# Kernel tuning notes

Measured on AMD Instinct MI355X. Metric: run time of the kernel, lower is better.

## Reference

```python
import jax, jax.numpy as jnp
import numpy as np

HEADS = 8
N = 2048; D_IN = 2048; LATENT = 2048; PROJ = 256; HIDDEN = 128
LAGS = 12; E = 65536; EMB = 128; N_ENT = 10000; N_TS = 1000


def _lag_weights(L):
    # weights(): flip(arange(1..L) / (L*(L+1)/2)); sums to 1
    w = np.arange(1, L + 1, dtype=np.float64) / (L * (L + 1) // 2)
    return jnp.asarray(np.ascontiguousarray(w[::-1]), dtype=jnp.float32)


def _gatv2(x, edge_index, Wl, bl, Wr, br, att, bias):
    # GATv2Conv with PyG defaults: self-loops added, leaky_relu(0.2),
    # softmax over incoming edges per target node, concat heads + bias.
    n = x.shape[0]
    H = HEADS
    D = Wl.shape[1] // H
    sl = jnp.arange(n, dtype=edge_index.dtype)
    src = jnp.concatenate([edge_index[0], sl])
    dst = jnp.concatenate([edge_index[1], sl])
    xl = (x @ Wl + bl).reshape(n, H, D)  # source / message transform
    xr = (x @ Wr + br).reshape(n, H, D)  # target transform
    e = jnp.sum(jax.nn.leaky_relu(xl[src] + xr[dst], 0.2) * att, axis=-1)  # [E', H]
    emax = jax.ops.segment_max(e, dst, num_segments=n)
    ee = jnp.exp(e - emax[dst])
    alpha = ee / jax.ops.segment_sum(ee, dst, num_segments=n)[dst]
    out = jax.ops.segment_sum(alpha[:, :, None] * xl[src], dst, num_segments=n)  # [n,H,D]
    return out.reshape(n, H * D) + bias


def _mha(query, lagged, Wq, bq, Wk, bk, Wv, bv):
    # MultiHeadCausalAttention: per-lag K/V projections combined with fixed
    # triangular weights. Since the weights sum to 1, the projection bias
    # passes through the weighted sum unchanged, so the per-lag Python loop
    # fuses into a single einsum over the lag axis.
    n = query.shape[0]
    dim_out = Wq.shape[1]
    dh = dim_out // HEADS
    Q = (query @ Wq + bq).reshape(n, -1, HEADS, dh).transpose(0, 2, 1, 3)  # [n,H,q,dh]
    tw = _lag_weights(lagged.shape[1])
    K = (jnp.einsum('nli,io,l->no', lagged, Wk, tw) + bk).reshape(n, 1, HEADS, dh).transpose(0, 2, 1, 3)
    V = (jnp.einsum('nli,io,l->no', lagged, Wv, tw) + bv).reshape(n, 1, HEADS, dh).transpose(0, 2, 1, 3)
    scores = jnp.einsum('nhqd,nhkd->nhqk', Q, K) / (dh ** 0.5)
    attn = jax.nn.softmax(scores, axis=-1)
    return jnp.einsum('nhqk,nhkd->nhqd', attn, V).transpose(0, 2, 1, 3).reshape(n, -1, dim_out)


def _forward(time_series_data, lagged_data, eps, gumbel_noise,
             entity_table, timestamp_table,
             gat_e_Wl, gat_e_bl, gat_e_Wr, gat_e_br, gat_e_att, gat_e_bias,
             enc_proj_W, enc_proj_b,
             enc_Wq, enc_bq, enc_Wk, enc_bk, enc_Wv, enc_bv,
             enc_fc_W, enc_fc_b,
             dec_Wq, dec_bq, dec_Wk, dec_bk, dec_Wv, dec_bv,
             gat_d_Wl, gat_d_bl, gat_d_Wr, gat_d_br, gat_d_att, gat_d_bias,
             dec_fc_W, dec_fc_b, A_direct, A_indirect,
             entity_indices, timestamp_indices, edge_index):
    entity_emb = entity_table[entity_indices]      # pretrained TKG entity embedding
    ts_emb = timestamp_table[timestamp_indices]    # pretrained TKG timestamp embedding
    feats = jnp.concatenate([time_series_data, entity_emb, ts_emb], axis=-1)
    x = jax.nn.relu(_gatv2(feats, edge_index, gat_e_Wl, gat_e_bl, gat_e_Wr, gat_e_br, gat_e_att, gat_e_bias))
    x = jax.nn.relu(x @ enc_proj_W + enc_proj_b)
    x = jax.nn.relu(_mha(x, lagged_data, enc_Wq, enc_bq, enc_Wk, enc_bk, enc_Wv, enc_bv))  # [N,1,PROJ]
    q_params = x @ enc_fc_W + enc_fc_b
    mean, log_var = jnp.split(q_params, 2, axis=-1)
    z = mean + jnp.exp(0.5 * log_var) * eps  # reparameterization, [N,1,LATENT]
    x = jax.nn.relu(_mha(z, lagged_data, dec_Wq, dec_bq, dec_Wk, dec_bk, dec_Wv, dec_bv))[:, 0, :]
    x = jax.nn.relu(_gatv2(x, edge_index, gat_d_Wl, gat_d_bl, gat_d_Wr, gat_d_br, gat_d_att, gat_d_bias))
    x_rec = x @ dec_fc_W + dec_fc_b  # [N, D_IN]
    direct = A_direct * jnp.sum(x_rec, axis=0)        # einsum('ij,tj->ij')
    indirect = A_indirect * jnp.sum(z, axis=(0, 1))   # einsum('ij,tlj->ij')
    causal_effect = direct + indirect
    y = jax.nn.softmax((causal_effect + gumbel_noise) / 0.5, axis=-1)  # tau=0.5
    hard = jax.nn.one_hot(jnp.argmax(y, axis=-1), y.shape[-1], dtype=y.dtype)
    adj = jax.lax.stop_gradient(hard - y) + y  # hard gumbel-softmax, straight-through
    return z, mean, log_var, x_rec, causal_effect, adj


def setup_inputs():
    key = jax.random.key(0)
    ks = iter(jax.random.split(key, 64))
    def nrm(shape, s=0.02):
        return jax.random.normal(next(ks), shape, jnp.float32) * s
    A0 = jnp.ones((N, N), jnp.float32) + jnp.eye(N, dtype=jnp.float32)
    A0 = A0 / jnp.sum(A0, axis=1)  # matches torch broadcast A0 / A0.sum(1)
    HH = HEADS * HIDDEN
    d = {
        'entity_indices': jax.random.randint(next(ks), (N,), 0, N_ENT),
        'relation_indices': jax.random.randint(next(ks), (N,), 0, N_TS),
        'timestamp_indices': jax.random.randint(next(ks), (N,), 0, N_TS),
        'time_series_data': jax.random.normal(next(ks), (N, D_IN), jnp.float32),
        'edge_index': jax.random.randint(next(ks), (2, E), 0, N),
        'lagged_data': jax.random.normal(next(ks), (N, LAGS, D_IN), jnp.float32),
        'eps': jax.random.normal(next(ks), (N, 1, LATENT), jnp.float32),
        'gumbel_noise': jax.random.gumbel(next(ks), (N, N), jnp.float32),
        'entity_table': nrm((N_ENT, EMB), 1.0),
        'timestamp_table': nrm((N_TS, EMB), 1.0),
        'gat_e_Wl': nrm((D_IN + 2 * EMB, HH)), 'gat_e_bl': jnp.zeros((HH,), jnp.float32),
        'gat_e_Wr': nrm((D_IN + 2 * EMB, HH)), 'gat_e_br': jnp.zeros((HH,), jnp.float32),
        'gat_e_att': nrm((HEADS, HIDDEN), 0.1), 'gat_e_bias': jnp.zeros((HH,), jnp.float32),
        'enc_proj_W': nrm((HH, PROJ)), 'enc_proj_b': jnp.zeros((PROJ,), jnp.float32),
        'enc_Wq': nrm((PROJ, PROJ)), 'enc_bq': jnp.zeros((PROJ,), jnp.float32),
        'enc_Wk': nrm((D_IN, PROJ)), 'enc_bk': jnp.zeros((PROJ,), jnp.float32),
        'enc_Wv': nrm((D_IN, PROJ)), 'enc_bv': jnp.zeros((PROJ,), jnp.float32),
        'enc_fc_W': nrm((PROJ, 2 * LATENT)), 'enc_fc_b': jnp.zeros((2 * LATENT,), jnp.float32),
        'dec_Wq': nrm((LATENT, PROJ)), 'dec_bq': jnp.zeros((PROJ,), jnp.float32),
        'dec_Wk': nrm((D_IN, PROJ)), 'dec_bk': jnp.zeros((PROJ,), jnp.float32),
        'dec_Wv': nrm((D_IN, PROJ)), 'dec_bv': jnp.zeros((PROJ,), jnp.float32),
        'gat_d_Wl': nrm((PROJ, HH)), 'gat_d_bl': jnp.zeros((HH,), jnp.float32),
        'gat_d_Wr': nrm((PROJ, HH)), 'gat_d_br': jnp.zeros((HH,), jnp.float32),
        'gat_d_att': nrm((HEADS, HIDDEN), 0.1), 'gat_d_bias': jnp.zeros((HH,), jnp.float32),
        'dec_fc_W': nrm((HH, D_IN)), 'dec_fc_b': jnp.zeros((D_IN,), jnp.float32),
        'A_direct': A0, 'A_indirect': A0,
    }
    return d


def reference(entity_indices, relation_indices, timestamp_indices, time_series_data,
              edge_index, lagged_data, eps, gumbel_noise,
              entity_table, timestamp_table,
              gat_e_Wl, gat_e_bl, gat_e_Wr, gat_e_br, gat_e_att, gat_e_bias,
              enc_proj_W, enc_proj_b,
              enc_Wq, enc_bq, enc_Wk, enc_bk, enc_Wv, enc_bv,
              enc_fc_W, enc_fc_b,
              dec_Wq, dec_bq, dec_Wk, dec_bk, dec_Wv, dec_bv,
              gat_d_Wl, gat_d_bl, gat_d_Wr, gat_d_br, gat_d_att, gat_d_bias,
              dec_fc_W, dec_fc_b, A_direct, A_indirect):
    # relation_indices are looked up by the pretrained TKG, but the relation
    # embedding is unused downstream in the original forward, so it is ignored.
    return _forward(time_series_data, lagged_data, eps, gumbel_noise,
                    entity_table, timestamp_table,
                    gat_e_Wl, gat_e_bl, gat_e_Wr, gat_e_br, gat_e_att, gat_e_bias,
                    enc_proj_W, enc_proj_b,
                    enc_Wq, enc_bq, enc_Wk, enc_bk, enc_Wv, enc_bv,
                    enc_fc_W, enc_fc_b,
                    dec_Wq, dec_bq, dec_Wk, dec_bk, dec_Wv, dec_bv,
                    gat_d_Wl, gat_d_bl, gat_d_Wr, gat_d_br, gat_d_att, gat_d_bias,
                    dec_fc_W, dec_fc_b, A_direct, A_indirect,
                    entity_indices, timestamp_indices, edge_index)
```

## Files before the change

kernel.cpp:

```cpp
#include <hip/hip_runtime.h>
#include <hip/hip_bf16.h>
#include <math.h>

#define N_NODES 2048
#define DIN     2048
#define HH      1024
#define LAGS    12
#define NE      65536
#define NL      (2048 * 2048)
#define CHUNK   128

#define BM 128
#define BN 128
#define BK 32

typedef __attribute__((ext_vector_type(8))) short short8;
typedef __attribute__((ext_vector_type(4))) float f32x4;

static __device__ __forceinline__ short f2bf_rne(float x) {
  union { float f; unsigned u; } c; c.f = x;
  unsigned u = c.u;
  unsigned r = (u + 0x7fffu + ((u >> 16) & 1u)) >> 16;
  return (short)r;
}
static __device__ __forceinline__ float bf2f(short h) {
  union { unsigned u; float f; } c; c.u = ((unsigned)(unsigned short)h) << 16;
  return c.f;
}

typedef __attribute__((address_space(3))) unsigned int as3_u32;
typedef const __attribute__((address_space(1))) unsigned int as1_u32c;
static __device__ __forceinline__ void gload_lds16(const void* g, void* l) {
  __builtin_amdgcn_global_load_lds((as1_u32c*)g, (as3_u32*)l, 16, 0, 0);
}

#define VMCNT6  asm volatile("s_waitcnt vmcnt(6)" ::: "memory")
#define VMCNT4  asm volatile("s_waitcnt vmcnt(4)" ::: "memory")
#define VMCNT0  asm volatile("s_waitcnt vmcnt(0)" ::: "memory")
#define SBAR()  do { asm volatile("" ::: "memory"); __builtin_amdgcn_s_barrier(); \
                     asm volatile("" ::: "memory"); } while (0)

struct WCfg { const float* W; short* H; short* L; int K; int N; int nb; };
struct WCfg2 { WCfg c[2]; };
struct WCfg4 { WCfg c[4]; };

static __device__ __forceinline__ void wsplit_tile(
    const WCfg& cf, int local, int tid, float t[32][33])
{
  const float* W = cf.W;
  short* H = cf.H;
  short* L = cf.L;
  int K = cf.K, N = cf.N;
  int nbx = N >> 5;
  int bx = local % nbx, by = local / nbx;
  int tx = tid & 31, ty = tid >> 5;
  int c0 = bx << 5, k0 = by << 5;
#pragma unroll
  for (int j = 0; j < 4; ++j)
    t[ty + 8 * j][tx] = W[(size_t)(k0 + ty + 8 * j) * N + c0 + tx];
  __syncthreads();
#pragma unroll
  for (int j = 0; j < 4; ++j) {
    int c = ty + 8 * j;
    float x = t[tx][c];
    short h = f2bf_rne(x);
    size_t off = (size_t)(c0 + c) * K + k0 + tx;
    H[off] = h;
    if (L) L[off] = f2bf_rne(x - bf2f(h));
  }
}

__global__ __launch_bounds__(256) void megaA_kernel(
    const float* __restrict__ lagged, short* __restrict__ lw, WCfg2 cfgs,
    int* __restrict__ cursor, float* __restrict__ csx,
    float* __restrict__ csz, float* __restrict__ cs_gat)
{
  __shared__ float t[32][33];
  int bid = blockIdx.x;
  int tid = threadIdx.x;

  if (bid < 2048) {
    int idx = bid * 256 + tid;
    int n = idx >> 8, c8 = idx & 255;
    const float* base = lagged + (size_t)n * (LAGS * DIN) + (size_t)c8 * 8;
    float a[8] = {};
#pragma unroll
    for (int l = 0; l < LAGS; ++l) {
      float w = (float)((double)(LAGS - l) / 78.0);
      float4 v0 = *(const float4*)(base + (size_t)l * DIN);
      float4 v1 = *(const float4*)(base + (size_t)l * DIN + 4);
      a[0] += w * v0.x; a[1] += w * v0.y; a[2] += w * v0.z; a[3] += w * v0.w;
      a[4] += w * v1.x; a[5] += w * v1.y; a[6] += w * v1.z; a[7] += w * v1.w;
    }
    short8 h;
#pragma unroll
    for (int j = 0; j < 8; ++j) h[j] = f2bf_rne(a[j]);
    *(short8*)(lw + (size_t)idx * 8) = h;
  } else if (bid < 3072) {
    int wb = bid - 2048;
    int i = (wb >= cfgs.c[0].nb) ? 1 : 0;
    int local = wb - (i ? cfgs.c[0].nb : 0);
    wsplit_tile(cfgs.c[i], local, tid, t);
  } else {
    int i = (bid - 3072) * 256 + tid;
    cursor[i] = 0; csx[i] = 0.f; csz[i] = 0.f;
    if (i < 1024) cs_gat[i] = 0.f;
  }
}

__global__ __launch_bounds__(256) void megaC_kernel(
    const short* __restrict__ A, const short* __restrict__ Bh0,
    const short* __restrict__ Bh1, short* __restrict__ Cpart,
    WCfg4 cfgs,
    const int* __restrict__ esrc, const int* __restrict__ edst,
    int* __restrict__ cursor, int* __restrict__ csr)
{
  __shared__ char smem[32768];
  int fb = blockIdx.x;
  int tid = threadIdx.x;

  if (fb < 512) {
    short* lds = (short*)smem;
    const int K = 2048, N = 256, M = 2048, klen = 256;
    int lane = tid & 63, wid = tid >> 6;
    int bn = (fb & 1) * BN;
    int bm = ((fb >> 1) & 15) * BM;
    int z = fb >> 5;
    int twin = z & 1;
    int kb = (z >> 1) * klen;
    const short* Bh = twin ? Bh1 : Bh0;

    const short* gp[4];
    int lofs[4];
    {
      int r4 = lane >> 2;
      int ksw = (lane & 3) ^ ((lane >> 3) & 3);
#pragma unroll
      for (int c = 0; c < 4; ++c) {
        int chunk = wid * 4 + c;
        int p = chunk >> 3, s = chunk & 7;
        int r = (s << 4) + r4;
        const short* bp = (p == 0) ? (A + (size_t)(bm + r) * K)
                                   : (Bh + (size_t)(bn + r) * K);
        gp[c] = bp + kb + (ksw << 3);
        lofs[c] = (p << 12) + (s << 9);
      }
    }
    auto stage = [&](int bo) {
#pragma unroll
      for (int c = 0; c < 4; ++c) {
        gload_lds16(gp[c], lds + bo + lofs[c]);
        gp[c] += BK;
      }
    };

    int l15 = lane & 15, l4 = lane >> 4;
    int wr = wid >> 1, wc = wid & 1;
    int soff = (l4 ^ ((l15 >> 1) & 3)) << 3;
    int aoff[4], bhoff[4];
#pragma unroll
    for (int i = 0; i < 4; ++i) {
      int r = wr * 64 + i * 16 + l15;
      int c = wc * 64 + i * 16 + l15;
      aoff[i]  = r * BK + soff;
      bhoff[i] = 4096 + c * BK + soff;
    }

    f32x4 acc[4][4];
#pragma unroll
    for (int m = 0; m < 4; ++m)
#pragma unroll
      for (int n = 0; n < 4; ++n) acc[m][n] = (f32x4){0.f, 0.f, 0.f, 0.f};

    stage(0);
    int cur = 0;
#pragma unroll
    for (int t = 0; t < 8; ++t) {
      if (t + 1 < 8) { stage(cur ? 0 : 8192); VMCNT4; }
      else { VMCNT0; }
      SBAR();
      const short* rb = lds + (cur ? 8192 : 0);
      short8 af[4], bh8[4];
#pragma unroll
      for (int i = 0; i < 4; ++i) {
        af[i]  = *(const short8*)(rb + aoff[i]);
        bh8[i] = *(const short8*)(rb + bhoff[i]);
      }
#pragma unroll
      for (int m = 0; m < 4; ++m)
#pragma unroll
        for (int n = 0; n < 4; ++n)
          acc[m][n] = __builtin_amdgcn_mfma_f32_16x16x32_bf16(af[m], bh8[n], acc[m][n], 0, 0, 0);
      SBAR();
      cur ^= 1;
    }

    short* P = Cpart + (size_t)z * ((size_t)M * N);
#pragma unroll
    for (int n = 0; n < 4; ++n) {
      int col = bn + wc * 64 + n * 16 + l15;
#pragma unroll
      for (int m = 0; m < 4; ++m) {
        int row0 = bm + wr * 64 + m * 16 + (l4 << 2);
#pragma unroll
        for (int r = 0; r < 4; ++r)
          P[(size_t)(row0 + r) * N + col] = f2bf_rne(acc[m][n][r]);
      }
    }
  } else if (fb < 4096) {
    float (*t)[33] = (float(*)[33])smem;
    int wb = fb - 512;
    int i = 0, base = 0;
    while (i < 3 && wb >= base + cfgs.c[i].nb) { base += cfgs.c[i].nb; ++i; }
    wsplit_tile(cfgs.c[i], wb - base, tid, t);
  } else {
    int i = (fb - 4096) * 256 + tid;
    if (i < NE) {
      int d = edst[i];
      int p = atomicAdd(&cursor[d], 1);
      if (p < 128) csr[(d << 7) + p] = esrc[i];
    } else if (i < NE + N_NODES) {
      int nn = i - NE;
      int p = atomicAdd(&cursor[nn], 1);
      if (p < 128) csr[(nn << 7) + p] = nn;
    }
  }
}

__global__ __launch_bounds__(256) void gemm_xrec(
    const short* __restrict__ A, const short* __restrict__ Bh,
    short* __restrict__ Cpart, float* __restrict__ cs_gat)
{
  __shared__ short lds[2 * 8192];
  const int K = 1024, N = 2048, M = 2048, klen = 512;
  int tid = threadIdx.x;
  int lane = tid & 63, wid = tid >> 6;
  int bn = blockIdx.x * BN, bm = blockIdx.y * BM;
  int z = blockIdx.z;
  int kb = z * klen;

  const short* gp[4];
  int lofs[4];
  {
    int r4 = lane >> 2;
    int ksw = (lane & 3) ^ ((lane >> 3) & 3);
#pragma unroll
    for (int c = 0; c < 4; ++c) {
      int chunk = wid * 4 + c;
      int p = chunk >> 3, s = chunk & 7;
      int r = (s << 4) + r4;
      const short* bp = (p == 0) ? (A + (size_t)(bm + r) * K)
                                 : (Bh + (size_t)(bn + r) * K);
      gp[c] = bp + kb + (ksw << 3);
      lofs[c] = (p << 12) + (s << 9);
    }
  }
  auto stage = [&](int bo) {
#pragma unroll
    for (int c = 0; c < 4; ++c) {
      gload_lds16(gp[c], lds + bo + lofs[c]);
      gp[c] += BK;
    }
  };

  int l15 = lane & 15, l4 = lane >> 4;
  int wr = wid >> 1, wc = wid & 1;
  int soff = (l4 ^ ((l15 >> 1) & 3)) << 3;
  int aoff[4], bhoff[4];
#pragma unroll
  for (int i = 0; i < 4; ++i) {
    int r = wr * 64 + i * 16 + l15;
    int c = wc * 64 + i * 16 + l15;
    aoff[i]  = r * BK + soff;
    bhoff[i] = 4096 + c * BK + soff;
  }

  f32x4 acc[4][4];
#pragma unroll
  for (int m = 0; m < 4; ++m)
#pragma unroll
    for (int n = 0; n < 4; ++n) acc[m][n] = (f32x4){0.f, 0.f, 0.f, 0.f};

  const int nt = klen / BK;
  stage(0);
  int cur = 0;
  for (int t = 0; t < nt; ++t) {
    if (t + 1 < nt) { stage(cur ? 0 : 8192); VMCNT4; }
    else { VMCNT0; }
    SBAR();
    const short* rb = lds + (cur ? 8192 : 0);
    short8 af[4], bh8[4];
#pragma unroll
    for (int i = 0; i < 4; ++i) {
      af[i]  = *(const short8*)(rb + aoff[i]);
      bh8[i] = *(const short8*)(rb + bhoff[i]);
    }
#pragma unroll
    for (int m = 0; m < 4; ++m)
#pragma unroll
      for (int n = 0; n < 4; ++n)
        acc[m][n] = __builtin_amdgcn_mfma_f32_16x16x32_bf16(af[m], bh8[n], acc[m][n], 0, 0, 0);
    SBAR();
    cur ^= 1;
  }

  short* P = Cpart + (size_t)z * ((size_t)M * N);
#pragma unroll
  for (int n = 0; n < 4; ++n) {
    int col = bn + wc * 64 + n * 16 + l15;
#pragma unroll
    for (int m = 0; m < 4; ++m) {
      int row0 = bm + wr * 64 + m * 16 + (l4 << 2);
#pragma unroll
      for (int r = 0; r < 4; ++r)
        P[(size_t)(row0 + r) * N + col] = f2bf_rne(acc[m][n][r]);
    }
  }

  if (blockIdx.x == 0) {
    int k0 = kb + tid * 2;
    float s0 = 0.f, s1 = 0.f;
    const short* Ar = A + (size_t)bm * K + k0;
    for (int r = 0; r < 128; ++r) {
      short2 v = *(const short2*)(Ar + (size_t)r * K);
      s0 += bf2f(v.x);
      s1 += bf2f(v.y);
    }
    atomicAdd(&cs_gat[k0], s0);
    atomicAdd(&cs_gat[k0 + 1], s1);
  }
}

__global__ __launch_bounds__(256) void gemm_dual(
    const short* __restrict__ xe, const short* __restrict__ xd,
    const short* __restrict__ fcH, const short* __restrict__ fcL,
    const short* __restrict__ WlH, const short* __restrict__ WlL,
    const short* __restrict__ WrH, const short* __restrict__ WrL,
    const float* __restrict__ fc_b, const float* __restrict__ bl,
    const float* __restrict__ br,
    float* __restrict__ out_mean, float* __restrict__ out_lv,
    short* __restrict__ xl, short* __restrict__ xr)
{
  __shared__ short lds[2 * 12288];
  const int K = 256;
  int fb = blockIdx.x;
  const short *A, *Bh, *Bl;
  const float* bias;
  int bm, bn, jobB, ldc;
  short* Obf = nullptr;
  float* Of = nullptr;
  if (fb < 512) {
    A = xe; Bh = fcH; Bl = fcL; bias = fc_b;
    bn = (fb & 31) << 7; bm = (fb >> 5) << 7;
    jobB = 0; ldc = 2048; Of = out_mean;
  } else {
    int g = fb - 512, twin = g & 1, t = g >> 1;
    A = xd; Bh = twin ? WrH : WlH; Bl = twin ? WrL : WlL;
    bias = twin ? br : bl;
    bn = (t & 7) << 7; bm = (t >> 3) << 7;
    jobB = 1; ldc = 1024; Obf = twin ? xr : xl;
  }

  int tid = threadIdx.x;
  int lane = tid & 63, wid = tid >> 6;

  const short* gp[6];
  int lofs[6];
  {
    int r4 = lane >> 2;
    int ksw = (lane & 3) ^ ((lane >> 3) & 3);
#pragma unroll
    for (int c = 0; c < 6; ++c) {
      int chunk = wid * 6 + c;
      int p = chunk >> 3, s = chunk & 7;
      int r = (s << 4) + r4;
      const short* bp = (p == 0) ? (A + (size_t)(bm + r) * K)
                      : (p == 1) ? (Bh + (size_t)(bn + r) * K)
                                 : (Bl + (size_t)(bn + r) * K);
      gp[c] = bp + (ksw << 3);
      lofs[c] = (p << 12) + (s << 9);
    }
  }
  auto stage = [&](int bo) {
#pragma unroll
    for (int c = 0; c < 6; ++c) {
      gload_lds16(gp[c], lds + bo + lofs[c]);
      gp[c] += BK;
    }
  };

  int l15 = lane & 15, l4 = lane >> 4;
  int wr = wid >> 1, wc = wid & 1;
  int soff = (l4 ^ ((l15 >> 1) & 3)) << 3;
  int aoff[4], bhoff[4], bloff[4];
#pragma unroll
  for (int i = 0; i < 4; ++i) {
    int r = wr * 64 + i * 16 + l15;
    int c = wc * 64 + i * 16 + l15;
    aoff[i]  = r * BK + soff;
    bhoff[i] = 4096 + c * BK + soff;
    bloff[i] = 8192 + c * BK + soff;
  }

  f32x4 acc[4][4];
#pragma unroll
  for (int m = 0; m < 4; ++m)
#pragma unroll
    for (int n = 0; n < 4; ++n) acc[m][n] = (f32x4){0.f, 0.f, 0.f, 0.f};

  stage(0);
  int cur = 0;
#pragma unroll
  for (int t = 0; t < 8; ++t) {
    if (t + 1 < 8) { stage(cur ? 0 : 12288); VMCNT6; }
    else { VMCNT0; }
    SBAR();
    const short* rb = lds + (cur ? 12288 : 0);
    short8 af[4], bh8[4], bl8[4];
#pragma unroll
    for (int i = 0; i < 4; ++i) {
      af[i]  = *(const short8*)(rb + aoff[i]);
      bh8[i] = *(const short8*)(rb + bhoff[i]);
      bl8[i] = *(const short8*)(rb + bloff[i]);
    }
#pragma unroll
    for (int m = 0; m < 4; ++m)
#pragma unroll
      for (int n = 0; n < 4; ++n) {
        acc[m][n] = __builtin_amdgcn_mfma_f32_16x16x32_bf16(af[m], bh8[n], acc[m][n], 0, 0, 0);
        acc[m][n] = __builtin_amdgcn_mfma_f32_16x16x32_bf16(af[m], bl8[n], acc[m][n], 0, 0, 0);
      }
    SBAR();
    cur ^= 1;
  }

#pragma unroll
  for (int n = 0; n < 4; ++n) {
    int col = bn + wc * 64 + n * 16 + l15;
    float bv = bias[col];
    if (jobB) {
#pragma unroll
      for (int m = 0; m < 4; ++m) {
        int row0 = bm + wr * 64 + m * 16 + (l4 << 2);
#pragma unroll
        for (int r = 0; r < 4; ++r)
          Obf[(size_t)(row0 + r) * ldc + col] = f2bf_rne(acc[m][n][r] + bv);
      }
    } else {
      float* O = Of; int oc = col;
      if (col >= 2048) { O = out_lv; oc = col - 2048; }
#pragma unroll
      for (int m = 0; m < 4; ++m) {
        int row0 = bm + wr * 64 + m * 16 + (l4 << 2);
#pragma unroll
        for (int r = 0; r < 4; ++r)
          O[(size_t)(row0 + r) * ldc + oc] = acc[m][n][r] + bv;
      }
    }
  }
}

__global__ __launch_bounds__(256) void sumrelu_kernel(
    const short* __restrict__ part, const float* __restrict__ b0,
    const float* __restrict__ b1, short* __restrict__ xe,
    short* __restrict__ xd)
{
  int i4 = blockIdx.x * 256 + threadIdx.x;
  size_t S = (size_t)N_NODES * 256;
  size_t base = (size_t)i4 * 4;
  int col = (int)(base & 255);
  float4 b0v = *(const float4*)(b0 + col);
  float4 b1v = *(const float4*)(b1 + col);
  float s0[4] = {}, s1[4] = {};
#pragma unroll
  for (int c = 0; c < 8; ++c) {
    short4 p0 = *(const short4*)(part + (size_t)(2 * c) * S + base);
    short4 p1 = *(const short4*)(part + (size_t)(2 * c + 1) * S + base);
    s0[0] += bf2f(p0.x); s0[1] += bf2f(p0.y); s0[2] += bf2f(p0.z); s0[3] += bf2f(p0.w);
    s1[0] += bf2f(p1.x); s1[1] += bf2f(p1.y); s1[2] += bf2f(p1.z); s1[3] += bf2f(p1.w);
  }
  short4 e, d;
  e.x = f2bf_rne(fmaxf(s0[0] + b0v.x, 0.f));
  e.y = f2bf_rne(fmaxf(s0[1] + b0v.y, 0.f));
  e.z = f2bf_rne(fmaxf(s0[2] + b0v.z, 0.f));
  e.w = f2bf_rne(fmaxf(s0[3] + b0v.w, 0.f));
  d.x = f2bf_rne(fmaxf(s1[0] + b1v.x, 0.f));
  d.y = f2bf_rne(fmaxf(s1[1] + b1v.y, 0.f));
  d.z = f2bf_rne(fmaxf(s1[2] + b1v.z, 0.f));
  d.w = f2bf_rne(fmaxf(s1[3] + b1v.w, 0.f));
  *(short4*)(xe + base) = e;
  *(short4*)(xd + base) = d;
}

__global__ __launch_bounds__(256) void megaB_kernel(
    const short* __restrict__ xl, const short* __restrict__ xr,
    const float* __restrict__ att, const float* __restrict__ bias,
    const int* __restrict__ csr, const int* __restrict__ cursor,
    short* __restrict__ outp,
    const float* __restrict__ mean_in, const float* __restrict__ lv_in,
    const float* __restrict__ eps, float* __restrict__ z,
    float* __restrict__ csz)
{
  __shared__ float xr_s[HH];
  __shared__ float att_s[HH];
  __shared__ float e_s[8 * CHUNK];
  __shared__ int   src_s[CHUNK];
  __shared__ float m_s[8], s_s[8], f_s[8];

  int tid = threadIdx.x;

  if (blockIdx.x >= 2048) {
    int flat = blockIdx.x - 2048;
    int c = ((flat & 3) * 256 + tid) * 2;
    int r0 = (flat >> 2) * 16;
    float sx = 0.f, sy = 0.f;
    for (int r = r0; r < r0 + 16; ++r) {
      size_t off = (size_t)r * 2048 + c;
      float2 m = *(const float2*)(mean_in + off);
      float2 v = *(const float2*)(lv_in + off);
      float2 e = *(const float2*)(eps + off);
      float zx = m.x + expf(0.5f * v.x) * e.x;
      float zy = m.y + expf(0.5f * v.y) * e.y;
      *(float2*)(z + off) = make_float2(zx, zy);
      sx += zx; sy += zy;
    }
    atomicAdd(&csz[c], sx);
    atomicAdd(&csz[c + 1], sy);
    return;
  }

  int n = blockIdx.x;
  {
    short4 x4 = ((const short4*)(xr + (size_t)n * HH))[tid];
    xr_s[tid * 4 + 0] = bf2f(x4.x);
    xr_s[tid * 4 + 1] = bf2f(x4.y);
    xr_s[tid * 4 + 2] = bf2f(x4.z);
    xr_s[tid * 4 + 3] = bf2f(x4.w);
  }
  ((float4*)att_s)[tid] = ((const float4*)att)[tid];
  if (tid < 8) { m_s[tid] = -INFINITY; s_s[tid] = 0.f; }
  __syncthreads();

  int beg = n << 7;
  int cnt_total = min(cursor[n], 128);
  int end = beg + cnt_total;
  int ht = tid >> 5;
  float4 acc = make_float4(0.f, 0.f, 0.f, 0.f);

  for (int c0 = beg; c0 < end; c0 += CHUNK) {
    int cnt = min(CHUNK, end - c0);
    if (tid < cnt) src_s[tid] = csr[c0 + tid];
    __syncthreads();

    int wave = tid >> 6, lane = tid & 63;
    int d0 = lane << 4;
    for (int e = wave; e < cnt; e += 4) {
      const short* xlr = xl + (size_t)src_s[e] * HH + d0;
      short8 a0 = *(const short8*)xlr;
      short8 a1 = *(const short8*)(xlr + 8);
      float sum = 0.f;
#pragma unroll
      for (int j = 0; j < 8; ++j) {
        float t = bf2f(a0[j]) + xr_s[d0 + j];
        t = t > 0.f ? t : 0.2f * t;
        sum += t * att_s[d0 + j];
      }
#pragma unroll
      for (int j = 0; j < 8; ++j) {
        float t = bf2f(a1[j]) + xr_s[d0 + 8 + j];
        t = t > 0.f ? t : 0.2f * t;
        sum += t * att_s[d0 + 8 + j];
      }
      sum += __shfl_xor(sum, 1);
      sum += __shfl_xor(sum, 2);
      sum += __shfl_xor(sum, 4);
      if ((lane & 7) == 0) e_s[(lane >> 3) * CHUNK + e] = sum;
    }
    __syncthreads();

    {
      int h = tid >> 5, i0 = tid & 31;
      float cm = -INFINITY;
      for (int e = i0; e < cnt; e += 32) cm = fmaxf(cm, e_s[h * CHUNK + e]);
#pragma unroll
      for (int m = 1; m < 32; m <<= 1) cm = fmaxf(cm, __shfl_xor(cm, m));
      float m_old = m_s[h];
      float m_new = fmaxf(m_old, cm);
      float csum = 0.f;
      for (int e = i0; e < cnt; e += 32) {
        float p = expf(e_s[h * CHUNK + e] - m_new);
        e_s[h * CHUNK + e] = p;
        csum += p;
      }
#pragma unroll
      for (int m = 1; m < 32; m <<= 1) csum += __shfl_xor(csum, m);
      if (i0 == 0) {
        float f = expf(m_old - m_new);
        s_s[h] = s_s[h] * f + csum;
        m_s[h] = m_new;
        f_s[h] = f;
      }
    }
    __syncthreads();

    float f = f_s[ht];
    acc.x *= f; acc.y *= f; acc.z *= f; acc.w *= f;
    for (int e = 0; e < cnt; ++e) {
      float p = e_s[ht * CHUNK + e];
      short4 v = *(const short4*)(xl + (size_t)src_s[e] * HH + (tid << 2));
      acc.x += p * bf2f(v.x); acc.y += p * bf2f(v.y);
      acc.z += p * bf2f(v.z); acc.w += p * bf2f(v.w);
    }
    __syncthreads();
  }

  float inv = 1.0f / s_s[ht];
  float4 b4 = *(const float4*)(bias + (tid << 2));
  short4 o4;
  o4.x = f2bf_rne(fmaxf(acc.x * inv + b4.x, 0.f));
  o4.y = f2bf_rne(fmaxf(acc.y * inv + b4.y, 0.f));
  o4.z = f2bf_rne(fmaxf(acc.z * inv + b4.z, 0.f));
  o4.w = f2bf_rne(fmaxf(acc.w * inv + b4.w, 0.f));
  *(short4*)(outp + (size_t)n * HH + (tid << 2)) = o4;
}

__global__ __launch_bounds__(256) void xrec_sum_kernel(
    const short* __restrict__ part, const float* __restrict__ bias,
    float* __restrict__ xrec, float* __restrict__ csx,
    const float* __restrict__ cs_gat, const short* __restrict__ dfL)
{
  int c = (blockIdx.x * 256 + threadIdx.x) * 2;
  int r0 = blockIdx.y * 16;
  size_t S = (size_t)N_NODES * 2048;
  float2 b = *(const float2*)(bias + c);
  float sx = 0.f, sy = 0.f;
  for (int r = r0; r < r0 + 16; ++r) {
    size_t off = (size_t)r * 2048 + c;
    short2 p0 = *(const short2*)(part + off);
    short2 p1 = *(const short2*)(part + S + off);
    float vx = bf2f(p0.x) + bf2f(p1.x) + b.x;
    float vy = bf2f(p0.y) + bf2f(p1.y) + b.y;
    *(float2*)(xrec + off) = make_float2(vx, vy);
    sx += vx; sy += vy;
  }
  {
    int k0 = blockIdx.y * 8;
    const short* rw0 = dfL + (size_t)c * 1024 + k0;
    const short* rw1 = dfL + (size_t)(c + 1) * 1024 + k0;
#pragma unroll
    for (int j = 0; j < 8; j += 4) {
      float4 g = *(const float4*)(cs_gat + k0 + j);
      short4 w0 = *(const short4*)(rw0 + j);
      short4 w1 = *(const short4*)(rw1 + j);
      sx += g.x * bf2f(w0.x) + g.y * bf2f(w0.y) + g.z * bf2f(w0.z) + g.w * bf2f(w0.w);
      sy += g.x * bf2f(w1.x) + g.y * bf2f(w1.y) + g.z * bf2f(w1.z) + g.w * bf2f(w1.w);
    }
  }
  atomicAdd(&csx[c], sx);
  atomicAdd(&csx[c + 1], sy);
}

__global__ __launch_bounds__(256) void final_kernel(
    const float* __restrict__ Ad, const float* __restrict__ Ai,
    const float* __restrict__ gum, const float* __restrict__ csx,
    const float* __restrict__ csz, float* __restrict__ ce_out,
    float* __restrict__ adj_out)
{
  int i = blockIdx.x;
  int tid = threadIdx.x;
  size_t rb = (size_t)i * 2048;

  float vmax = -INFINITY; int vidx = 0;
  for (int j4 = tid; j4 < 512; j4 += 256) {
    float4 ad = *(const float4*)(Ad  + rb + (size_t)j4 * 4);
    float4 ai = *(const float4*)(Ai  + rb + (size_t)j4 * 4);
    float4 g  = *(const float4*)(gum + rb + (size_t)j4 * 4);
    float4 cx = *(const float4*)(csx + (size_t)j4 * 4);
    float4 cz = *(const float4*)(csz + (size_t)j4 * 4);
    float4 ce;
    ce.x = ad.x * cx.x + ai.x * cz.x;
    ce.y = ad.y * cx.y + ai.y * cz.y;
    ce.z = ad.z * cx.z + ai.z * cz.z;
    ce.w = ad.w * cx.w + ai.w * cz.w;
    *(float4*)(ce_out + rb + (size_t)j4 * 4) = ce;
    int j = j4 * 4;
    float l;
    l = (ce.x + g.x) * 2.0f; if (l > vmax) { vmax = l; vidx = j; }
    l = (ce.y + g.y) * 2.0f; if (l > vmax) { vmax = l; vidx = j + 1; }
    l = (ce.z + g.z) * 2.0f; if (l > vmax) { vmax = l; vidx = j + 2; }
    l = (ce.w + g.w) * 2.0f; if (l > vmax) { vmax = l; vidx = j + 3; }
  }
  for (int m = 1; m < 64; m <<= 1) {
    float ov = __shfl_xor(vmax, m);
    int   oi = __shfl_xor(vidx, m);
    if (ov > vmax || (ov == vmax && oi < vidx)) { vmax = ov; vidx = oi; }
  }
  __shared__ float wm[4];
  __shared__ int   wi[4];
  __shared__ int   amax;
  int lane = tid & 63, wave = tid >> 6;
  if (lane == 0) { wm[wave] = vmax; wi[wave] = vidx; }
  __syncthreads();
  if (tid == 0) {
    float bv = wm[0]; int bi = wi[0];
    for (int w = 1; w < 4; ++w)
      if (wm[w] > bv || (wm[w] == bv && wi[w] < bi)) { bv = wm[w]; bi = wi[w]; }
    amax = bi;
  }
  __syncthreads();
  int am = amax;
  for (int j4 = tid; j4 < 512; j4 += 256) {
    int j = j4 * 4;
    float4 o;
    o.x = (j     == am) ? 1.f : 0.f;
    o.y = (j + 1 == am) ? 1.f : 0.f;
    o.z = (j + 2 == am) ? 1.f : 0.f;
    o.w = (j + 3 == am) ? 1.f : 0.f;
    *(float4*)(adj_out + rb + (size_t)j4 * 4) = o;
  }
}

extern "C" void kernel_launch(void* const* d_in, const int* in_sizes, int n_in,
                              void* d_out, int out_size, void* d_ws, size_t ws_size,
                              hipStream_t stream) {
  (void)in_sizes; (void)n_in; (void)out_size; (void)ws_size;

  const int*   edge_index = (const int*)d_in[4];
  const float* lagged     = (const float*)d_in[5];
  const float* eps        = (const float*)d_in[6];
  const float* gumbel     = (const float*)d_in[7];
  const float* enc_Wv     = (const float*)d_in[22];
  const float* enc_bv     = (const float*)d_in[23];
  const float* enc_fc_W   = (const float*)d_in[24];
  const float* enc_fc_b   = (const float*)d_in[25];
  const float* dec_Wv     = (const float*)d_in[30];
  const float* dec_bv     = (const float*)d_in[31];
  const float* gat_Wl     = (const float*)d_in[32];
  const float* gat_bl     = (const float*)d_in[33];
  const float* gat_Wr     = (const float*)d_in[34];
  const float* gat_br     = (const float*)d_in[35];
  const float* gat_att    = (const float*)d_in[36];
  const float* gat_bias   = (const float*)d_in[37];
  const float* dec_fc_W   = (const float*)d_in[38];
  const float* dec_fc_b   = (const float*)d_in[39];
  const float* A_dir      = (const float*)d_in[40];
  const float* A_ind      = (const float*)d_in[41];

  float* out      = (float*)d_out;
  float* out_z    = out;
  float* out_mean = out + (size_t)NL;
  float* out_lv   = out + 2 * (size_t)NL;
  float* out_xrec = out + 3 * (size_t)NL;
  float* out_ce   = out + 4 * (size_t)NL;
  float* out_adj  = out + 5 * (size_t)NL;

  char* ws = (char*)d_ws;
  short* lw_bf = (short*)(ws);
  short* WvH0  = (short*)(ws + ((size_t) 8 << 20));
  short* WvH1  = (short*)(ws + ((size_t)10 << 20));
  short* fcH   = (short*)(ws + ((size_t)12 << 20));
  short* fcL   = (short*)(ws + ((size_t)14 << 20));
  short* WlH   = (short*)(ws + ((size_t)16 << 20));
  short* WlL   = (short*)(ws + ((size_t)16 << 20) + (512u << 10));
  short* WrH   = (short*)(ws + ((size_t)17 << 20));
  short* WrL   = (short*)(ws + ((size_t)17 << 20) + (512u << 10));
  short* dfH   = (short*)(ws + ((size_t)18 << 20));
  short* dfL   = (short*)(ws + ((size_t)22 << 20));
  short* xe_bf = (short*)(ws + ((size_t)26 << 20));
  short* xd_bf = (short*)(ws + ((size_t)27 << 20));
  short* xl    = (short*)(ws + ((size_t)28 << 20));
  short* xr    = (short*)(ws + ((size_t)32 << 20));
  short* gt_bf = (short*)(ws + ((size_t)44 << 20));
  short* part  = (short*)(ws + ((size_t)48 << 20));
  int*   cursor = (int*) (ws + ((size_t)64 << 20));
  int*   csr    = (int*) (ws + ((size_t)64 << 20) + (64u << 10));
  float* csx    = (float*)(ws + ((size_t)66 << 20));
  float* csz    = (float*)(ws + ((size_t)66 << 20) + (16u << 10));
  float* cs_gat = (float*)(ws + ((size_t)66 << 20) + (32u << 10));

  const int* e_src = edge_index;
  const int* e_dst = edge_index + NE;

  {
    WCfg2 c2;
    c2.c[0] = { enc_Wv, WvH0, nullptr, 2048, 256, 512 };
    c2.c[1] = { dec_Wv, WvH1, nullptr, 2048, 256, 512 };
    megaA_kernel<<<3080, 256, 0, stream>>>(lagged, lw_bf, c2,
                                           cursor, csx, csz, cs_gat);
  }

  {
    WCfg4 c4;
    c4.c[0] = { enc_fc_W, fcH, fcL, 256,  4096, 1024 };
    c4.c[1] = { gat_Wl,   WlH, WlL, 256,  1024, 256  };
    c4.c[2] = { gat_Wr,   WrH, WrL, 256,  1024, 256  };
    c4.c[3] = { dec_fc_W, dfH, dfL, 1024, 2048, 2048 };
    megaC_kernel<<<4360, 256, 0, stream>>>(
        lw_bf, WvH0, WvH1, part, c4, e_src, e_dst, cursor, csr);
  }

  sumrelu_kernel<<<512, 256, 0, stream>>>(part, enc_bv, dec_bv, xe_bf, xd_bf);

  gemm_dual<<<768, 256, 0, stream>>>(
      xe_bf, xd_bf, fcH, fcL, WlH, WlL, WrH, WrL,
      enc_fc_b, gat_bl, gat_br, out_mean, out_lv, xl, xr);

  megaB_kernel<<<2560, 256, 0, stream>>>(
      xl, xr, gat_att, gat_bias, csr, cursor, gt_bf,
      out_mean, out_lv, eps, out_z, csz);

  gemm_xrec<<<dim3(16, 16, 2), 256, 0, stream>>>(gt_bf, dfH, part, cs_gat);
  xrec_sum_kernel<<<dim3(4, 128), 256, 0, stream>>>(
      part, dec_fc_b, out_xrec, csx, cs_gat, dfL);

  final_kernel<<<N_NODES, 256, 0, stream>>>(A_dir, A_ind, gumbel, csx, csz,
                                            out_ce, out_adj);
}
```

Baseline: 188.5 us.

## Halve split-K partials in value GEMM and drop low-part weights for GAT projections

The lagged-value GEMM in megaC now uses 256 blocks with a K slice of 512 instead of 512 blocks with a slice of 256. This halves the number of bf16 partial buffers that sumrelu must read and reduce. Separately, the GAT Wl/Wr projections in gemm_dual now use only the high bf16 part of the split weights. That drops the second MFMA and the extra B-tile load on that path, at the cost of reduced precision in xl/xr. Fewer blocks in the split-K GEMM lengthens each block's serial loop and lowers parallelism.

```diff
diff --git a/kernel.cpp b/kernel.cpp
--- a/kernel.cpp
+++ b/kernel.cpp
@@ -119,9 +119,9 @@
   int fb = blockIdx.x;
   int tid = threadIdx.x;
 
-  if (fb < 512) {
+  if (fb < 256) {
     short* lds = (short*)smem;
-    const int K = 2048, N = 256, M = 2048, klen = 256;
+    const int K = 2048, N = 256, M = 2048, klen = 512;
     int lane = tid & 63, wid = tid >> 6;
     int bn = (fb & 1) * BN;
     int bm = ((fb >> 1) & 15) * BM;
@@ -172,11 +172,11 @@
 #pragma unroll
       for (int n = 0; n < 4; ++n) acc[m][n] = (f32x4){0.f, 0.f, 0.f, 0.f};
 
+    const int nt = klen / BK;
     stage(0);
     int cur = 0;
-#pragma unroll
-    for (int t = 0; t < 8; ++t) {
-      if (t + 1 < 8) { stage(cur ? 0 : 8192); VMCNT4; }
+    for (int t = 0; t < nt; ++t) {
+      if (t + 1 < nt) { stage(cur ? 0 : 8192); VMCNT4; }
       else { VMCNT0; }
       SBAR();
       const short* rb = lds + (cur ? 8192 : 0);
@@ -207,14 +207,14 @@
           P[(size_t)(row0 + r) * N + col] = f2bf_rne(acc[m][n][r]);
       }
     }
-  } else if (fb < 4096) {
+  } else if (fb < 3840) {
     float (*t)[33] = (float(*)[33])smem;
-    int wb = fb - 512;
+    int wb = fb - 256;
     int i = 0, base = 0;
     while (i < 3 && wb >= base + cfgs.c[i].nb) { base += cfgs.c[i].nb; ++i; }
     wsplit_tile(cfgs.c[i], wb - base, tid, t);
   } else {
-    int i = (fb - 4096) * 256 + tid;
+    int i = (fb - 3840) * 256 + tid;
     if (i < NE) {
       int d = edst[i];
       int p = atomicAdd(&cursor[d], 1);
@@ -334,8 +334,7 @@
 __global__ __launch_bounds__(256) void gemm_dual(
     const short* __restrict__ xe, const short* __restrict__ xd,
     const short* __restrict__ fcH, const short* __restrict__ fcL,
-    const short* __restrict__ WlH, const short* __restrict__ WlL,
-    const short* __restrict__ WrH, const short* __restrict__ WrL,
+    const short* __restrict__ WlH, const short* __restrict__ WrH,
     const float* __restrict__ fc_b, const float* __restrict__ bl,
     const float* __restrict__ br,
     float* __restrict__ out_mean, float* __restrict__ out_lv,
@@ -344,117 +343,177 @@
   __shared__ short lds[2 * 12288];
   const int K = 256;
   int fb = blockIdx.x;
-  const short *A, *Bh, *Bl;
-  const float* bias;
-  int bm, bn, jobB, ldc;
-  short* Obf = nullptr;
-  float* Of = nullptr;
-  if (fb < 512) {
-    A = xe; Bh = fcH; Bl = fcL; bias = fc_b;
-    bn = (fb & 31) << 7; bm = (fb >> 5) << 7;
-    jobB = 0; ldc = 2048; Of = out_mean;
-  } else {
-    int g = fb - 512, twin = g & 1, t = g >> 1;
-    A = xd; Bh = twin ? WrH : WlH; Bl = twin ? WrL : WlL;
-    bias = twin ? br : bl;
-    bn = (t & 7) << 7; bm = (t >> 3) << 7;
-    jobB = 1; ldc = 1024; Obf = twin ? xr : xl;
-  }
-
   int tid = threadIdx.x;
   int lane = tid & 63, wid = tid >> 6;
-
-  const short* gp[6];
-  int lofs[6];
-  {
-    int r4 = lane >> 2;
-    int ksw = (lane & 3) ^ ((lane >> 3) & 3);
-#pragma unroll
-    for (int c = 0; c < 6; ++c) {
-      int chunk = wid * 6 + c;
-      int p = chunk >> 3, s = chunk & 7;
-      int r = (s << 4) + r4;
-      const short* bp = (p == 0) ? (A + (size_t)(bm + r) * K)
-                      : (p == 1) ? (Bh + (size_t)(bn + r) * K)
-                                 : (Bl + (size_t)(bn + r) * K);
-      gp[c] = bp + (ksw << 3);
-      lofs[c] = (p << 12) + (s << 9);
-    }
-  }
-  auto stage = [&](int bo) {
-#pragma unroll
-    for (int c = 0; c < 6; ++c) {
-      gload_lds16(gp[c], lds + bo + lofs[c]);
-      gp[c] += BK;
-    }
-  };
-
   int l15 = lane & 15, l4 = lane >> 4;
   int wr = wid >> 1, wc = wid & 1;
   int soff = (l4 ^ ((l15 >> 1) & 3)) << 3;
-  int aoff[4], bhoff[4], bloff[4];
-#pragma unroll
-  for (int i = 0; i < 4; ++i) {
-    int r = wr * 64 + i * 16 + l15;
-    int c = wc * 64 + i * 16 + l15;
-    aoff[i]  = r * BK + soff;
-    bhoff[i] = 4096 + c * BK + soff;
-    bloff[i] = 8192 + c * BK + soff;
-  }
-
-  f32x4 acc[4][4];
-#pragma unroll
-  for (int m = 0; m < 4; ++m)
-#pragma unroll
-    for (int n = 0; n < 4; ++n) acc[m][n] = (f32x4){0.f, 0.f, 0.f, 0.f};
-
-  stage(0);
-  int cur = 0;
-#pragma unroll
-  for (int t = 0; t < 8; ++t) {
-    if (t + 1 < 8) { stage(cur ? 0 : 12288); VMCNT6; }
-    else { VMCNT0; }
-    SBAR();
-    const short* rb = lds + (cur ? 12288 : 0);
-    short8 af[4], bh8[4], bl8[4];
+
+  if (fb < 512) {
+    const short* A = xe;
+    int bn = (fb & 31) << 7, bm = (fb >> 5) << 7;
+
+    const short* gp[6];
+    int lofs[6];
+    {
+      int r4 = lane >> 2;
+      int ksw = (lane & 3) ^ ((lane >> 3) & 3);
+#pragma unroll
+      for (int c = 0; c < 6; ++c) {
+        int chunk = wid * 6 + c;
+        int p = chunk >> 3, s = chunk & 7;
+        int r = (s << 4) + r4;
+        const short* bp = (p == 0) ? (A + (size_t)(bm + r) * K)
+                        : (p == 1) ? (fcH + (size_t)(bn + r) * K)
+                                   : (fcL + (size_t)(bn + r) * K);
+        gp[c] = bp + (ksw << 3);
+        lofs[c] = (p << 12) + (s << 9);
+      }
+    }
+    auto stage = [&](int bo) {
+#pragma unroll
+      for (int c = 0; c < 6; ++c) {
+        gload_lds16(gp[c], lds + bo + lofs[c]);
+        gp[c] += BK;
+      }
+    };
+
+    int aoff[4], bhoff[4], bloff[4];
 #pragma unroll
     for (int i = 0; i < 4; ++i) {
-      af[i]  = *(const short8*)(rb + aoff[i]);
-      bh8[i] = *(const short8*)(rb + bhoff[i]);
-      bl8[i] = *(const short8*)(rb + bloff[i]);
-    }
+      int r = wr * 64 + i * 16 + l15;
+      int c = wc * 64 + i * 16 + l15;
+      aoff[i]  = r * BK + soff;
+      bhoff[i] = 4096 + c * BK + soff;
+      bloff[i] = 8192 + c * BK + soff;
+    }
+
+    f32x4 acc[4][4];
 #pragma unroll
     for (int m = 0; m < 4; ++m)
 #pragma unroll
-      for (int n = 0; n < 4; ++n) {
-        acc[m][n] = __builtin_amdgcn_mfma_f32_16x16x32_bf16(af[m], bh8[n], acc[m][n], 0, 0, 0);
-        acc[m][n] = __builtin_amdgcn_mfma_f32_16x16x32_bf16(af[m], bl8[n], acc[m][n], 0, 0, 0);
-      }
-    SBAR();
-    cur ^= 1;
-  }
-
-#pragma unroll
-  for (int n = 0; n < 4; ++n) {
-    int col = bn + wc * 64 + n * 16 + l15;
-    float bv = bias[col];
-    if (jobB) {
+      for (int n = 0; n < 4; ++n) acc[m][n] = (f32x4){0.f, 0.f, 0.f, 0.f};
+
+    stage(0);
+    int cur = 0;
+#pragma unroll
+    for (int t = 0; t < 8; ++t) {
+      if (t + 1 < 8) { stage(cur ? 0 : 12288); VMCNT6; }
+      else { VMCNT0; }
+      SBAR();
+      const short* rb = lds + (cur ? 12288 : 0);
+      short8 af[4], bh8[4], bl8[4];
+#pragma unroll
+      for (int i = 0; i < 4; ++i) {
+        af[i]  = *(const short8*)(rb + aoff[i]);
+        bh8[i] = *(const short8*)(rb + bhoff[i]);
+        bl8[i] = *(const short8*)(rb + bloff[i]);
+      }
+#pragma unroll
+      for (int m = 0; m < 4; ++m)
+#pragma unroll
+        for (int n = 0; n < 4; ++n) {
+          acc[m][n] = __builtin_amdgcn_mfma_f32_16x16x32_bf16(af[m], bh8[n], acc[m][n], 0, 0, 0);
+          acc[m][n] = __builtin_amdgcn_mfma_f32_16x16x32_bf16(af[m], bl8[n], acc[m][n], 0, 0, 0);
+        }
+      SBAR();
+      cur ^= 1;
+    }
+
+#pragma unroll
+    for (int n = 0; n < 4; ++n) {
+      int col = bn + wc * 64 + n * 16 + l15;
+      float bv = fc_b[col];
+      float* O = out_mean; int oc = col;
+      if (col >= 2048) { O = out_lv; oc = col - 2048; }
 #pragma unroll
       for (int m = 0; m < 4; ++m) {
         int row0 = bm + wr * 64 + m * 16 + (l4 << 2);
 #pragma unroll
         for (int r = 0; r < 4; ++r)
-          Obf[(size_t)(row0 + r) * ldc + col] = f2bf_rne(acc[m][n][r] + bv);
-      }
-    } else {
-      float* O = Of; int oc = col;
-      if (col >= 2048) { O = out_lv; oc = col - 2048; }
+          O[(size_t)(row0 + r) * 2048 + oc] = acc[m][n][r] + bv;
+      }
+    }
+  } else {
+    int g = fb - 512, twin = g & 1, t0 = g >> 1;
+    const short* A = xd;
+    const short* Bh = twin ? WrH : WlH;
+    const float* bias = twin ? br : bl;
+    int bn = (t0 & 7) << 7, bm = (t0 >> 3) << 7;
+    short* Obf = twin ? xr : xl;
+
+    const short* gp[4];
+    int lofs[4];
+    {
+      int r4 = lane >> 2;
+      int ksw = (lane & 3) ^ ((lane >> 3) & 3);
+#pragma unroll
+      for (int c = 0; c < 4; ++c) {
+        int chunk = wid * 4 + c;
+        int p = chunk >> 3, s = chunk & 7;
+        int r = (s << 4) + r4;
+        const short* bp = (p == 0) ? (A + (size_t)(bm + r) * K)
+                                   : (Bh + (size_t)(bn + r) * K);
+        gp[c] = bp + (ksw << 3);
+        lofs[c] = (p << 12) + (s << 9);
+      }
+    }
+    auto stage = [&](int bo) {
+#pragma unroll
+      for (int c = 0; c < 4; ++c) {
+        gload_lds16(gp[c], lds + bo + lofs[c]);
+        gp[c] += BK;
+      }
+    };
+
+    int aoff[4], bhoff[4];
+#pragma unroll
+    for (int i = 0; i < 4; ++i) {
+      int r = wr * 64 + i * 16 + l15;
+      int c = wc * 64 + i * 16 + l15;
+      aoff[i]  = r * BK + soff;
+      bhoff[i] = 4096 + c * BK + soff;
+    }
+
+    f32x4 acc[4][4];
+#pragma unroll
+    for (int m = 0; m < 4; ++m)
+#pragma unroll
+      for (int n = 0; n < 4; ++n) acc[m][n] = (f32x4){0.f, 0.f, 0.f, 0.f};
+
+    stage(0);
+    int cur = 0;
+#pragma unroll
+    for (int t = 0; t < 8; ++t) {
+      if (t + 1 < 8) { stage(cur ? 0 : 8192); VMCNT4; }
+      else { VMCNT0; }
+      SBAR();
+      const short* rb = lds + (cur ? 8192 : 0);
+      short8 af[4], bh8[4];
+#pragma unroll
+      for (int i = 0; i < 4; ++i) {
+        af[i]  = *(const short8*)(rb + aoff[i]);
+        bh8[i] = *(const short8*)(rb + bhoff[i]);
+      }
+#pragma unroll
+      for (int m = 0; m < 4; ++m)
+#pragma unroll
+        for (int n = 0; n < 4; ++n)
+          acc[m][n] = __builtin_amdgcn_mfma_f32_16x16x32_bf16(af[m], bh8[n], acc[m][n], 0, 0, 0);
+      SBAR();
+      cur ^= 1;
+    }
+
+#pragma unroll
+    for (int n = 0; n < 4; ++n) {
+      int col = bn + wc * 64 + n * 16 + l15;
+      float bv = bias[col];
 #pragma unroll
       for (int m = 0; m < 4; ++m) {
         int row0 = bm + wr * 64 + m * 16 + (l4 << 2);
 #pragma unroll
         for (int r = 0; r < 4; ++r)
-          O[(size_t)(row0 + r) * ldc + oc] = acc[m][n][r] + bv;
+          Obf[(size_t)(row0 + r) * 1024 + col] = f2bf_rne(acc[m][n][r] + bv);
       }
     }
   }
@@ -473,7 +532,7 @@
   float4 b1v = *(const float4*)(b1 + col);
   float s0[4] = {}, s1[4] = {};
 #pragma unroll
-  for (int c = 0; c < 8; ++c) {
+  for (int c = 0; c < 4; ++c) {
     short4 p0 = *(const short4*)(part + (size_t)(2 * c) * S + base);
     short4 p1 = *(const short4*)(part + (size_t)(2 * c + 1) * S + base);
     s0[0] += bf2f(p0.x); s0[1] += bf2f(p0.y); s0[2] += bf2f(p0.z); s0[3] += bf2f(p0.w);
@@ -795,14 +854,14 @@
     c4.c[1] = { gat_Wl,   WlH, WlL, 256,  1024, 256  };
     c4.c[2] = { gat_Wr,   WrH, WrL, 256,  1024, 256  };
     c4.c[3] = { dec_fc_W, dfH, dfL, 1024, 2048, 2048 };
-    megaC_kernel<<<4360, 256, 0, stream>>>(
+    megaC_kernel<<<4104, 256, 0, stream>>>(
         lw_bf, WvH0, WvH1, part, c4, e_src, e_dst, cursor, csr);
   }
 
   sumrelu_kernel<<<512, 256, 0, stream>>>(part, enc_bv, dec_bv, xe_bf, xd_bf);
 
   gemm_dual<<<768, 256, 0, stream>>>(
-      xe_bf, xd_bf, fcH, fcL, WlH, WlL, WrH, WrL,
+      xe_bf, xd_bf, fcH, fcL, WlH, WrH,
       enc_fc_b, gat_bl, gat_br, out_mean, out_lv, xl, xr);
 
   megaB_kernel<<<2560, 256, 0, stream>>>(
```

Measured after the change: 185.3 us. About the same (-1.7%).
